# Performance work log

Measured on AMD Instinct MI355X. Metric: run time of the kernel, lower is better.

The kernel has to match this reference:

```python
import jax, jax.numpy as jnp
import numpy as np

VOCAB = 100000
DIM = 128
B = 16384
K = 20
INITRANGE = 0.5 / DIM


def setup_inputs() -> dict:
    key = jax.random.key(0)
    k1, k2, k3, k4 = jax.random.split(key, 4)
    u_emb = jax.random.uniform(k1, (VOCAB, DIM), dtype=jnp.float32,
                               minval=-INITRANGE, maxval=INITRANGE)
    v_emb = jnp.zeros((VOCAB, DIM), dtype=jnp.float32)
    u_pos = jax.random.randint(k2, (B,), 0, VOCAB, dtype=jnp.int64)
    v_pos = jax.random.randint(k3, (B,), 0, VOCAB, dtype=jnp.int64)
    v_neg = jax.random.randint(k4, (B, K), 0, VOCAB, dtype=jnp.int64)
    return {"u_emb": u_emb, "v_emb": v_emb, "u_pos": u_pos,
            "v_pos": v_pos, "v_neg": v_neg, "batch_size": B}


def reference(u_emb, v_emb, u_pos, v_pos, v_neg, batch_size):
    embed_u = u_emb[u_pos]                      # [B, D]
    embed_v = v_emb[v_pos]                      # [B, D]
    score = jnp.sum(embed_u * embed_v, axis=1)  # [B]
    log_target = jax.nn.log_sigmoid(score)      # [B]
    neg_embed_v = v_emb[v_neg]                  # [B, K, D]
    # bmm([B,K,D], [B,D,1]) -> [B,K]
    neg_score = jnp.einsum('bkd,bd->bk', neg_embed_v, embed_u)
    neg_score = jnp.sum(neg_score, axis=1)      # [B]
    sum_log_sampled = jax.nn.log_sigmoid(-neg_score)
    loss = log_target + sum_log_sampled
    return -jnp.sum(loss) / batch_size
```

## Files before the change

kernel.cpp:

```cpp
#include <hip/hip_runtime.h>
#include <hip/hip_bf16.h>

#define DIM   128
#define KNEG  20

__device__ __forceinline__ float log_sigmoid(float x) {
    float ax = fabsf(x);
    float t = log1pf(__expf(-ax));
    return (x >= 0.0f) ? -t : (x - t);
}

__global__ __launch_bounds__(256) void skipgram_loss_kernel(
    const float* __restrict__ u_emb,
    const float* __restrict__ v_emb,
    const int* __restrict__ u_pos,
    const int* __restrict__ v_pos,
    const int* __restrict__ v_neg,
    float* __restrict__ acc,
    int B_total)
{
    const int lane  = threadIdx.x & 63;
    const int wib   = threadIdx.x >> 6;
    const int wave  = blockIdx.x * 4 + wib;
    const int nwave = gridDim.x * 4;
    const int col   = lane * 2;

    float local = 0.0f;

    for (int b = wave; b < B_total; b += nwave) {
        const int ui = u_pos[b];
        const int vi = v_pos[b];

        const float2 uu = *(const float2*)(u_emb + (size_t)ui * DIM + col);

        const float2 vv = *(const float2*)(v_emb + (size_t)vi * DIM + col);
        float p = uu.x * vv.x + uu.y * vv.y;

        int nidx[KNEG];
        #pragma unroll
        for (int k = 0; k < KNEG; ++k) nidx[k] = v_neg[b * KNEG + k];

        float ns0 = 0.0f, ns1 = 0.0f;
        #pragma unroll
        for (int k = 0; k < KNEG; ++k) {
            const float2 nv = *(const float2*)(v_emb + (size_t)nidx[k] * DIM + col);
            ns0 += nv.x;
            ns1 += nv.y;
        }
        float nd = uu.x * ns0 + uu.y * ns1;

        #pragma unroll
        for (int off = 32; off > 0; off >>= 1) {
            p  += __shfl_xor(p,  off, 64);
            nd += __shfl_xor(nd, off, 64);
        }

        if (lane == 0) {
            local += log_sigmoid(p) + log_sigmoid(-nd);
        }
    }

    __shared__ float sbuf[4];
    if (lane == 0) sbuf[wib] = local;
    __syncthreads();
    if (threadIdx.x == 0) {
        float s = sbuf[0] + sbuf[1] + sbuf[2] + sbuf[3];
        atomicAdd(acc, s);
    }
}

__global__ void finalize_kernel(const float* __restrict__ acc,
                                const int* __restrict__ batch_size,
                                float* __restrict__ out)
{
    out[0] = -acc[0] / (float)batch_size[0];
}

extern "C" void kernel_launch(void* const* d_in, const int* in_sizes, int n_in,
                              void* d_out, int out_size, void* d_ws, size_t ws_size,
                              hipStream_t stream) {
    const float* u_emb = (const float*)d_in[0];
    const float* v_emb = (const float*)d_in[1];
    const int* u_pos = (const int*)d_in[2];
    const int* v_pos = (const int*)d_in[3];
    const int* v_neg = (const int*)d_in[4];
    const int* bsz   = (const int*)d_in[5];

    const int B_total = in_sizes[2];

    float* acc = (float*)d_ws;
    hipMemsetAsync(acc, 0, sizeof(float), stream);

    const int blocks = 1024;
    skipgram_loss_kernel<<<blocks, 256, 0, stream>>>(
        u_emb, v_emb, u_pos, v_pos, v_neg, acc, B_total);

    finalize_kernel<<<1, 1, 0, stream>>>(acc, bsz, (float*)d_out);
}
```

Baseline: 138.9 us.

## Use one wave per sample with float4 half-wave row gathers and partials reduction

Each wave now handles exactly one batch element, with a grid sized to the batch instead of a grid-stride loop. The 22 indices are loaded in parallel, one per lane, and broadcast with shuffles. Each half-wave fetches one 128-float row as float4, so two rows are in flight per instruction and the serial per-lane index loads go away. Per-block partials are written to workspace and summed by a 256-thread finalize kernel, which replaces the atomicAdd and the memset. This trades more blocks and a larger partial-sum buffer for better memory-level parallelism.

```diff
diff --git a/kernel.cpp b/kernel.cpp
--- a/kernel.cpp
+++ b/kernel.cpp
@@ -16,64 +16,84 @@
     const int* __restrict__ u_pos,
     const int* __restrict__ v_pos,
     const int* __restrict__ v_neg,
-    float* __restrict__ acc,
+    float* __restrict__ partials,
     int B_total)
 {
-    const int lane  = threadIdx.x & 63;
-    const int wib   = threadIdx.x >> 6;
-    const int wave  = blockIdx.x * 4 + wib;
-    const int nwave = gridDim.x * 4;
-    const int col   = lane * 2;
+    const int lane = threadIdx.x & 63;
+    const int wib  = threadIdx.x >> 6;
+    const int b    = blockIdx.x * 4 + wib;
+    const int half = lane >> 5;
+    const int l32  = lane & 31;
+    const int col  = l32 * 4;
+
+    float p = 0.0f;
+    float nd = 0.0f;
+
+    if (b < B_total) {
+        int myidx = 0;
+        if (lane == 0)           myidx = v_pos[b];
+        else if (lane <= KNEG)   myidx = v_neg[b * KNEG + lane - 1];
+        else if (lane == 21)     myidx = u_pos[b];
+
+        const int ui = __shfl(myidx, 21, 64);
+        const float4 U = *(const float4*)(u_emb + (size_t)ui * DIM + col);
+
+        float4 ns = make_float4(0.f, 0.f, 0.f, 0.f);
+        #pragma unroll
+        for (int i = 0; i < 11; ++i) {
+            const int r  = 2 * i + half;
+            const int rr = (r <= KNEG) ? r : KNEG;
+            const int idx = __shfl(myidx, rr, 64);
+            const float4 row = *(const float4*)(v_emb + (size_t)idx * DIM + col);
+            if (r == 0) {
+                p = U.x * row.x + U.y * row.y + U.z * row.z + U.w * row.w;
+            } else if (r <= KNEG) {
+                ns.x += row.x; ns.y += row.y; ns.z += row.z; ns.w += row.w;
+            }
+        }
+        nd = U.x * ns.x + U.y * ns.y + U.z * ns.z + U.w * ns.w;
+    }
+
+    #pragma unroll
+    for (int off = 32; off > 0; off >>= 1) {
+        p  += __shfl_xor(p,  off, 64);
+        nd += __shfl_xor(nd, off, 64);
+    }
 
     float local = 0.0f;
-
-    for (int b = wave; b < B_total; b += nwave) {
-        const int ui = u_pos[b];
-        const int vi = v_pos[b];
-
-        const float2 uu = *(const float2*)(u_emb + (size_t)ui * DIM + col);
-
-        const float2 vv = *(const float2*)(v_emb + (size_t)vi * DIM + col);
-        float p = uu.x * vv.x + uu.y * vv.y;
-
-        int nidx[KNEG];
-        #pragma unroll
-        for (int k = 0; k < KNEG; ++k) nidx[k] = v_neg[b * KNEG + k];
-
-        float ns0 = 0.0f, ns1 = 0.0f;
-        #pragma unroll
-        for (int k = 0; k < KNEG; ++k) {
-            const float2 nv = *(const float2*)(v_emb + (size_t)nidx[k] * DIM + col);
-            ns0 += nv.x;
-            ns1 += nv.y;
-        }
-        float nd = uu.x * ns0 + uu.y * ns1;
-
-        #pragma unroll
-        for (int off = 32; off > 0; off >>= 1) {
-            p  += __shfl_xor(p,  off, 64);
-            nd += __shfl_xor(nd, off, 64);
-        }
-
-        if (lane == 0) {
-            local += log_sigmoid(p) + log_sigmoid(-nd);
-        }
+    if (lane == 0 && b < B_total) {
+        local = log_sigmoid(p) + log_sigmoid(-nd);
     }
 
     __shared__ float sbuf[4];
     if (lane == 0) sbuf[wib] = local;
     __syncthreads();
     if (threadIdx.x == 0) {
-        float s = sbuf[0] + sbuf[1] + sbuf[2] + sbuf[3];
-        atomicAdd(acc, s);
+        partials[blockIdx.x] = sbuf[0] + sbuf[1] + sbuf[2] + sbuf[3];
     }
 }
 
-__global__ void finalize_kernel(const float* __restrict__ acc,
-                                const int* __restrict__ batch_size,
-                                float* __restrict__ out)
+__global__ __launch_bounds__(256) void finalize_kernel(
+    const float* __restrict__ partials, int n,
+    const int* __restrict__ batch_size,
+    float* __restrict__ out)
 {
-    out[0] = -acc[0] / (float)batch_size[0];
+    const int lane = threadIdx.x & 63;
+    const int wib  = threadIdx.x >> 6;
+
+    float s = 0.0f;
+    for (int i = threadIdx.x; i < n; i += 256) s += partials[i];
+
+    #pragma unroll
+    for (int off = 32; off > 0; off >>= 1) s += __shfl_xor(s, off, 64);
+
+    __shared__ float sbuf[4];
+    if (lane == 0) sbuf[wib] = s;
+    __syncthreads();
+    if (threadIdx.x == 0) {
+        float total = sbuf[0] + sbuf[1] + sbuf[2] + sbuf[3];
+        out[0] = -total / (float)batch_size[0];
+    }
 }
 
 extern "C" void kernel_launch(void* const* d_in, const int* in_sizes, int n_in,
@@ -87,13 +107,12 @@
     const int* bsz   = (const int*)d_in[5];
 
     const int B_total = in_sizes[2];
+    const int blocks  = (B_total + 3) / 4;
 
-    float* acc = (float*)d_ws;
-    hipMemsetAsync(acc, 0, sizeof(float), stream);
+    float* partials = (float*)d_ws;
 
-    const int blocks = 1024;
     skipgram_loss_kernel<<<blocks, 256, 0, stream>>>(
-        u_emb, v_emb, u_pos, v_pos, v_neg, acc, B_total);
+        u_emb, v_emb, u_pos, v_pos, v_neg, partials, B_total);
 
-    finalize_kernel<<<1, 1, 0, stream>>>(acc, bsz, (float*)d_out);
+    finalize_kernel<<<1, 256, 0, stream>>>(partials, blocks, bsz, (float*)d_out);
 }
```

Result: faster. 135.4 us (-2.5%).
